# Kernel tuning notes

Hardware: AMD Instinct MI355X
Metric: run time of the kernel (lower is better)

## Reference

```python
import jax, jax.numpy as jnp
import numpy as np

B, T, V, E, H, O = 512, 64, 1024, 256, 512, 256


def setup_inputs() -> dict:
    key = jax.random.key(0)
    ks = jax.random.split(key, 9)
    s = 0.02
    return {
        "message": jax.random.normal(ks[0], (B, T, V), jnp.float32),
        "W_emb": jax.random.normal(ks[1], (E, V), jnp.float32) * s,   # Linear(vocab, embed).weight
        "b_emb": jnp.zeros((E,), jnp.float32),
        "W_ih": jax.random.normal(ks[2], (4 * H, E), jnp.float32) * s,  # LSTMCell weight_ih (i,f,g,o)
        "b_ih": jnp.zeros((4 * H,), jnp.float32),
        "W_hh": jax.random.normal(ks[3], (4 * H, H), jnp.float32) * s,  # LSTMCell weight_hh
        "b_hh": jnp.zeros((4 * H,), jnp.float32),
        "W_agent": jax.random.normal(ks[4], (O, H), jnp.float32) * s,   # agent Linear(hidden, out)
        "b_agent": jnp.zeros((O,), jnp.float32),
    }


def reference(message, W_emb, b_emb, W_ih, b_ih, W_hh, b_hh, W_agent, b_agent):
    # Embedding for all timesteps at once: [B,T,V] @ [E,V]^T -> [B,T,E]
    emb = jnp.einsum('btv,ev->bte', message, W_emb) + b_emb
    # Precompute input-side gate preactivations for every step: [B,T,4H]
    x_gates = jnp.einsum('bte,ge->btg', emb, W_ih) + (b_ih + b_hh)
    x_gates = jnp.swapaxes(x_gates, 0, 1)  # [T,B,4H] for scan
    Bsz = message.shape[0]
    Hh = W_hh.shape[1]

    def step(carry, xg):
        h, c = carry
        g = xg + h @ W_hh.T                      # [B,4H]
        i, f, gg, o = jnp.split(g, 4, axis=-1)   # PyTorch LSTMCell gate order i,f,g,o
        i = jax.nn.sigmoid(i)
        f = jax.nn.sigmoid(f)
        gg = jnp.tanh(gg)
        o = jax.nn.sigmoid(o)
        c = f * c + i * gg
        h = o * jnp.tanh(c)
        return (h, c), h

    h0 = jnp.zeros((Bsz, Hh), message.dtype)
    _, hs = jax.lax.scan(step, (h0, h0), x_gates)  # hs: [T,B,H]
    # Agent head applied to every step's hidden state, output [B,T,O]
    out = jnp.einsum('tbh,oh->bto', hs, W_agent) + b_agent
    return out
```

## Files before the change

kernel.cpp:

```cpp
#include <hip/hip_runtime.h>

typedef unsigned short u16;
typedef unsigned int u32;
typedef unsigned long long u64;
typedef __attribute__((ext_vector_type(8))) short bf16x8;
typedef __attribute__((ext_vector_type(4))) float f32x4;

__device__ inline u16 f2bf(float x) {
  u32 u = __float_as_uint(x);
  u32 r = (u + 0x7FFFu + ((u >> 16) & 1u)) >> 16;
  return (u16)r;
}
__device__ inline float bf2f(u16 h) { return __uint_as_float(((u32)h) << 16); }
__device__ inline float sigm(float x) { return 1.f / (1.f + __expf(-x)); }
__device__ inline float tanh_s(float x) {
  float ax = fabsf(x);
  float e = __expf(2.f * ax);
  float t = 1.f - 2.f / (e + 1.f);
  return copysignf(t, x);
}

__global__ void cvt_f32_bf16(const float* __restrict__ s, u16* __restrict__ d, int n) {
  int i = (blockIdx.x * 256 + threadIdx.x) * 4;
  if (i < n) {
    float4 f = *(const float4*)&s[i];
    u32 lo = (u32)f2bf(f.x) | ((u32)f2bf(f.y) << 16);
    u32 hi = (u32)f2bf(f.z) | ((u32)f2bf(f.w) << 16);
    uint2 v; v.x = lo; v.y = hi;
    *(uint2*)&d[i] = v;
  }
}

__global__ void bias_add(const float* __restrict__ a, const float* __restrict__ b,
                         float* __restrict__ d, int n) {
  int i = blockIdx.x * 256 + threadIdx.x;
  if (i < n) d[i] = a[i] + b[i];
}

__global__ void zero_u32(u32* __restrict__ p, int n) {
  int i = blockIdx.x * 256 + threadIdx.x;
  if (i < n) p[i] = 0;
}

template <int A_F32, int OUT_BF16>
__global__ __launch_bounds__(256) void gemm_bt(
    const void* __restrict__ Ap, const u16* __restrict__ Bp,
    const float* __restrict__ bias, void* __restrict__ Cp,
    int K, int lda, int ldb, int ldc) {
  __shared__ u16 Alds[128 * 64];
  __shared__ u16 Blds[128 * 64];
  const int tid = threadIdx.x;
  const int lane = tid & 63;
  const int w = tid >> 6;
  const int wm = w >> 1, wn = w & 1;
  const int m0 = blockIdx.x * 128, n0 = blockIdx.y * 128;
  const int r = lane & 15, kb = lane >> 4;

  f32x4 acc[4][4];
#pragma unroll
  for (int m = 0; m < 4; ++m)
#pragma unroll
    for (int n = 0; n < 4; ++n) acc[m][n] = (f32x4)0.f;

  for (int k0 = 0; k0 < K; k0 += 64) {
#pragma unroll
    for (int p = 0; p < 4; ++p) {
      int ch = p * 256 + tid;
      int row = ch >> 3;
      int col = (ch & 7) * 8;
      int scol = col ^ ((row & 7) << 3);
      if (A_F32) {
        const float* s = (const float*)Ap + (size_t)(m0 + row) * lda + k0 + col;
        float4 f0 = *(const float4*)s;
        float4 f1 = *(const float4*)(s + 4);
        uint4 v;
        v.x = (u32)f2bf(f0.x) | ((u32)f2bf(f0.y) << 16);
        v.y = (u32)f2bf(f0.z) | ((u32)f2bf(f0.w) << 16);
        v.z = (u32)f2bf(f1.x) | ((u32)f2bf(f1.y) << 16);
        v.w = (u32)f2bf(f1.z) | ((u32)f2bf(f1.w) << 16);
        *(uint4*)&Alds[row * 64 + scol] = v;
      } else {
        uint4 v = *(const uint4*)((const u16*)Ap + (size_t)(m0 + row) * lda + k0 + col);
        *(uint4*)&Alds[row * 64 + scol] = v;
      }
      uint4 vb = *(const uint4*)(Bp + (size_t)(n0 + row) * ldb + k0 + col);
      *(uint4*)&Blds[row * 64 + scol] = vb;
    }
    __syncthreads();
#pragma unroll
    for (int ks = 0; ks < 2; ++ks) {
      int kk = ks * 32 + kb * 8;
      bf16x8 af[4], bfr[4];
#pragma unroll
      for (int m = 0; m < 4; ++m) {
        int row = wm * 64 + m * 16 + r;
        af[m] = *(const bf16x8*)&Alds[row * 64 + (kk ^ ((row & 7) << 3))];
      }
#pragma unroll
      for (int n = 0; n < 4; ++n) {
        int row = wn * 64 + n * 16 + r;
        bfr[n] = *(const bf16x8*)&Blds[row * 64 + (kk ^ ((row & 7) << 3))];
      }
#pragma unroll
      for (int m = 0; m < 4; ++m)
#pragma unroll
        for (int n = 0; n < 4; ++n)
          acc[m][n] = __builtin_amdgcn_mfma_f32_16x16x32_bf16(af[m], bfr[n], acc[m][n], 0, 0, 0);
    }
    __syncthreads();
  }

  const int r4 = kb * 4;
#pragma unroll
  for (int m = 0; m < 4; ++m) {
#pragma unroll
    for (int n = 0; n < 4; ++n) {
      int row = m0 + wm * 64 + m * 16 + r4;
      int col = n0 + wn * 64 + n * 16 + (lane & 15);
      float bv = bias[col];
#pragma unroll
      for (int j = 0; j < 4; ++j) {
        float v = acc[m][n][j] + bv;
        if (OUT_BF16)
          ((u16*)Cp)[(size_t)(row + j) * ldc + col] = f2bf(v);
        else
          ((float*)Cp)[(size_t)(row + j) * ldc + col] = v;
      }
    }
  }
}

__global__ __launch_bounds__(256, 1) void lstm_persist(
    const u16* __restrict__ xg,
    const u16* __restrict__ Whh,
    u16* __restrict__ h2,
    u16* __restrict__ hs,
    u32* ctr) {
  const int tid = threadIdx.x;
  const int lane = tid & 63;
  const int w = tid >> 6;
  const int g = blockIdx.x & 7;
  const int m = blockIdx.x >> 3;
  const int b0 = g * 64;
  const int hc0 = m * 16;
  const int col = lane & 15;
  const int q = lane >> 4;

  float cst[4] = {0.f, 0.f, 0.f, 0.f};
  const int arow = b0 + w * 16 + col;
  const int gr0 = b0 + w * 16 + q * 4;

  for (int t = 0; t < 64; ++t) {
    float xv[4][4];
#pragma unroll
    for (int j = 0; j < 4; ++j) {
      const u16* xp = xg + ((size_t)(gr0 + j) * 64 + t) * 2048 + hc0 + col;
#pragma unroll
      for (int n = 0; n < 4; ++n) xv[n][j] = bf2f(xp[n * 512]);
    }

    f32x4 acc[4];
#pragma unroll
    for (int n = 0; n < 4; ++n) acc[n] = (f32x4)0.f;

    if (t > 0) {
      const u16* hp = h2 + (size_t)((t - 1) & 1) * (512 * 512) + (size_t)arow * 512;
#pragma unroll
      for (int kf = 0; kf < 16; ++kf) {
        union { u64 qq[2]; bf16x8 v; } ua;
        const u64* hq = (const u64*)&hp[kf * 32 + q * 8];
        ua.qq[0] = __hip_atomic_load(&hq[0], __ATOMIC_RELAXED, __HIP_MEMORY_SCOPE_AGENT);
        ua.qq[1] = __hip_atomic_load(&hq[1], __ATOMIC_RELAXED, __HIP_MEMORY_SCOPE_AGENT);
#pragma unroll
        for (int n = 0; n < 4; ++n) {
          bf16x8 bfr = *(const bf16x8*)&Whh[(size_t)(n * 512 + hc0 + col) * 512 + kf * 32 + q * 8];
          acc[n] = __builtin_amdgcn_mfma_f32_16x16x32_bf16(ua.v, bfr, acc[n], 0, 0, 0);
        }
      }
    }

    u16* hw = h2 + (size_t)(t & 1) * (512 * 512);
#pragma unroll
    for (int j = 0; j < 4; ++j) {
      float vi = acc[0][j] + xv[0][j];
      float vf = acc[1][j] + xv[1][j];
      float vg = acc[2][j] + xv[2][j];
      float vo = acc[3][j] + xv[3][j];
      float ii = sigm(vi), ff = sigm(vf), gg = tanh_s(vg), oo = sigm(vo);
      float cn = ff * cst[j] + ii * gg;
      cst[j] = cn;
      u16 hb = f2bf(oo * tanh_s(cn));
      int br = gr0 + j;
      __hip_atomic_store(&hw[(size_t)br * 512 + hc0 + col], hb,
                         __ATOMIC_RELAXED, __HIP_MEMORY_SCOPE_AGENT);
      hs[((size_t)br * 64 + t) * 512 + hc0 + col] = hb;
    }

    if (t < 63) {
      asm volatile("s_waitcnt vmcnt(0)" ::: "memory");
      __syncthreads();
      if (tid == 0) {
        u32* c = &ctr[(size_t)(t * 8 + g) * 32];
        __hip_atomic_fetch_add(c, 1u, __ATOMIC_RELAXED, __HIP_MEMORY_SCOPE_AGENT);
        while (__hip_atomic_load(c, __ATOMIC_RELAXED, __HIP_MEMORY_SCOPE_AGENT) < 32u)
          __builtin_amdgcn_s_sleep(2);
      }
      __syncthreads();
    }
  }
}

extern "C" void kernel_launch(void* const* d_in, const int* in_sizes, int n_in,
                              void* d_out, int out_size, void* d_ws, size_t ws_size,
                              hipStream_t stream) {
  (void)in_sizes; (void)n_in; (void)out_size; (void)ws_size;
  const float* msg   = (const float*)d_in[0];
  const float* W_emb = (const float*)d_in[1];
  const float* b_emb = (const float*)d_in[2];
  const float* W_ih  = (const float*)d_in[3];
  const float* b_ih  = (const float*)d_in[4];
  const float* W_hh  = (const float*)d_in[5];
  const float* b_hh  = (const float*)d_in[6];
  const float* W_ag  = (const float*)d_in[7];
  const float* b_ag  = (const float*)d_in[8];
  float* out = (float*)d_out;

  char* p = (char*)d_ws;
  u16* Wemb_b = (u16*)p;  p += (size_t)256 * 1024 * 2;
  u16* Wih_b  = (u16*)p;  p += (size_t)2048 * 256 * 2;
  u16* Whh_b  = (u16*)p;  p += (size_t)2048 * 512 * 2;
  u16* Wag_b  = (u16*)p;  p += (size_t)256 * 512 * 2;
  float* bc   = (float*)p; p += (size_t)2048 * 4;
  p = (char*)(((size_t)p + 255) & ~(size_t)255);
  u16* emb_b = (u16*)p;   p += (size_t)32768 * 256 * 2;
  u16* xg    = (u16*)p;   p += (size_t)32768 * 2048 * 2;
  u16* hs    = (u16*)p;   p += (size_t)32768 * 512 * 2;
  u16* h2    = (u16*)p;   p += (size_t)2 * 512 * 512 * 2;
  u32* ctr   = (u32*)p;   p += (size_t)64 * 8 * 32 * 4;

  cvt_f32_bf16<<<256, 256, 0, stream>>>(W_emb, Wemb_b, 256 * 1024);
  cvt_f32_bf16<<<512, 256, 0, stream>>>(W_ih, Wih_b, 2048 * 256);
  cvt_f32_bf16<<<1024, 256, 0, stream>>>(W_hh, Whh_b, 2048 * 512);
  cvt_f32_bf16<<<128, 256, 0, stream>>>(W_ag, Wag_b, 256 * 512);
  bias_add<<<8, 256, 0, stream>>>(b_ih, b_hh, bc, 2048);
  zero_u32<<<64, 256, 0, stream>>>(ctr, 64 * 8 * 32);

  gemm_bt<1, 1><<<dim3(256, 2), 256, 0, stream>>>(msg, Wemb_b, b_emb, emb_b,
                                                  1024, 1024, 1024, 256);
  gemm_bt<0, 1><<<dim3(256, 16), 256, 0, stream>>>(emb_b, Wih_b, bc, xg,
                                                   256, 256, 256, 2048);
  lstm_persist<<<256, 256, 0, stream>>>(xg, Whh_b, h2, hs, ctr);
  gemm_bt<0, 0><<<dim3(256, 2), 256, 0, stream>>>(hs, Wag_b, b_ag, out,
                                                  512, 512, 512, 256);
}
```

Measured before the change: 1.132 ms.

## Stage W_hh and h in swizzled LDS, time-major gate layout, prefetch xgates

After: 1.036 ms. 8.5% less time.

```diff
diff --git a/kernel.cpp b/kernel.cpp
--- a/kernel.cpp
+++ b/kernel.cpp
@@ -42,7 +42,7 @@
   if (i < n) p[i] = 0;
 }
 
-template <int A_F32, int OUT_BF16>
+template <int A_F32, int OUT_BF16, int ROWPERM>
 __global__ __launch_bounds__(256) void gemm_bt(
     const void* __restrict__ Ap, const u16* __restrict__ Bp,
     const float* __restrict__ bias, void* __restrict__ Cp,
@@ -121,21 +121,25 @@
 #pragma unroll
       for (int j = 0; j < 4; ++j) {
         float v = acc[m][n][j] + bv;
+        size_t crow = ROWPERM ? ((size_t)((row + j) & 63) * 512 + ((row + j) >> 6))
+                              : (size_t)(row + j);
         if (OUT_BF16)
-          ((u16*)Cp)[(size_t)(row + j) * ldc + col] = f2bf(v);
+          ((u16*)Cp)[crow * ldc + col] = f2bf(v);
         else
-          ((float*)Cp)[(size_t)(row + j) * ldc + col] = v;
+          ((float*)Cp)[crow * ldc + col] = v;
       }
     }
   }
 }
 
 __global__ __launch_bounds__(256, 1) void lstm_persist(
-    const u16* __restrict__ xg,
+    const u16* __restrict__ xgT,
     const u16* __restrict__ Whh,
     u16* __restrict__ h2,
     u16* __restrict__ hs,
     u32* ctr) {
+  __shared__ u16 Bl[64 * 512];
+  __shared__ u16 hA[64 * 512];
   const int tid = threadIdx.x;
   const int lane = tid & 63;
   const int w = tid >> 6;
@@ -143,60 +147,97 @@
   const int m = blockIdx.x >> 3;
   const int b0 = g * 64;
   const int hc0 = m * 16;
-  const int col = lane & 15;
-  const int q = lane >> 4;
-
-  float cst[4] = {0.f, 0.f, 0.f, 0.f};
-  const int arow = b0 + w * 16 + col;
-  const int gr0 = b0 + w * 16 + q * 4;
+  const int r = lane & 15, q = lane >> 4;
+
+  {
+    int row = tid >> 2;
+    int gg = row >> 4, cc = row & 15;
+    int c0 = (tid & 3) * 128;
+    const u16* src = Whh + (size_t)(gg * 512 + hc0 + cc) * 512 + c0;
+#pragma unroll
+    for (int i = 0; i < 16; ++i) {
+      int col = c0 + i * 8;
+      int scol = col ^ ((row & 7) << 3);
+      *(uint4*)&Bl[row * 512 + scol] = *(const uint4*)&src[i * 8];
+    }
+  }
+  __syncthreads();
+
+  float cstate[4] = {0.f, 0.f, 0.f, 0.f};
+  const int bl0 = b0 + w * 16 + q * 4;
+
+  u16 xv[4][4];
+#pragma unroll
+  for (int j = 0; j < 4; ++j) {
+    const u16* xp = xgT + (size_t)(bl0 + j) * 2048 + hc0 + r;
+#pragma unroll
+    for (int n = 0; n < 4; ++n) xv[j][n] = xp[n * 512];
+  }
 
   for (int t = 0; t < 64; ++t) {
-    float xv[4][4];
+    f32x4 acc[4];
+#pragma unroll
+    for (int n = 0; n < 4; ++n) acc[n] = (f32x4)0.f;
+
+    if (t > 0) {
+      {
+        int row = tid >> 2;
+        int c0 = (tid & 3) * 128;
+        const u64* src = (const u64*)(h2 + (size_t)((t - 1) & 1) * (512 * 512) +
+                                      (size_t)(b0 + row) * 512 + c0);
+        u64 tmp[32];
+#pragma unroll
+        for (int i = 0; i < 32; ++i)
+          tmp[i] = __hip_atomic_load(&src[i], __ATOMIC_RELAXED, __HIP_MEMORY_SCOPE_AGENT);
+#pragma unroll
+        for (int i = 0; i < 16; ++i) {
+          int col = c0 + i * 8;
+          int scol = col ^ ((row & 7) << 3);
+          u64* dst = (u64*)&hA[row * 512 + scol];
+          dst[0] = tmp[i * 2];
+          dst[1] = tmp[i * 2 + 1];
+        }
+      }
+      __syncthreads();
+
+#pragma unroll
+      for (int kf = 0; kf < 16; ++kf) {
+        int k = kf * 32 + q * 8;
+        int scol = k ^ ((r & 7) << 3);
+        bf16x8 a = *(const bf16x8*)&hA[(w * 16 + r) * 512 + scol];
+#pragma unroll
+        for (int n = 0; n < 4; ++n) {
+          bf16x8 b = *(const bf16x8*)&Bl[(n * 16 + r) * 512 + scol];
+          acc[n] = __builtin_amdgcn_mfma_f32_16x16x32_bf16(a, b, acc[n], 0, 0, 0);
+        }
+      }
+    }
+
+    u16* hw = h2 + (size_t)(t & 1) * (512 * 512);
 #pragma unroll
     for (int j = 0; j < 4; ++j) {
-      const u16* xp = xg + ((size_t)(gr0 + j) * 64 + t) * 2048 + hc0 + col;
-#pragma unroll
-      for (int n = 0; n < 4; ++n) xv[n][j] = bf2f(xp[n * 512]);
-    }
-
-    f32x4 acc[4];
-#pragma unroll
-    for (int n = 0; n < 4; ++n) acc[n] = (f32x4)0.f;
-
-    if (t > 0) {
-      const u16* hp = h2 + (size_t)((t - 1) & 1) * (512 * 512) + (size_t)arow * 512;
-#pragma unroll
-      for (int kf = 0; kf < 16; ++kf) {
-        union { u64 qq[2]; bf16x8 v; } ua;
-        const u64* hq = (const u64*)&hp[kf * 32 + q * 8];
-        ua.qq[0] = __hip_atomic_load(&hq[0], __ATOMIC_RELAXED, __HIP_MEMORY_SCOPE_AGENT);
-        ua.qq[1] = __hip_atomic_load(&hq[1], __ATOMIC_RELAXED, __HIP_MEMORY_SCOPE_AGENT);
-#pragma unroll
-        for (int n = 0; n < 4; ++n) {
-          bf16x8 bfr = *(const bf16x8*)&Whh[(size_t)(n * 512 + hc0 + col) * 512 + kf * 32 + q * 8];
-          acc[n] = __builtin_amdgcn_mfma_f32_16x16x32_bf16(ua.v, bfr, acc[n], 0, 0, 0);
-        }
-      }
-    }
-
-    u16* hw = h2 + (size_t)(t & 1) * (512 * 512);
-#pragma unroll
-    for (int j = 0; j < 4; ++j) {
-      float vi = acc[0][j] + xv[0][j];
-      float vf = acc[1][j] + xv[1][j];
-      float vg = acc[2][j] + xv[2][j];
-      float vo = acc[3][j] + xv[3][j];
+      float vi = acc[0][j] + bf2f(xv[j][0]);
+      float vf = acc[1][j] + bf2f(xv[j][1]);
+      float vg = acc[2][j] + bf2f(xv[j][2]);
+      float vo = acc[3][j] + bf2f(xv[j][3]);
       float ii = sigm(vi), ff = sigm(vf), gg = tanh_s(vg), oo = sigm(vo);
-      float cn = ff * cst[j] + ii * gg;
-      cst[j] = cn;
+      float cn = ff * cstate[j] + ii * gg;
+      cstate[j] = cn;
       u16 hb = f2bf(oo * tanh_s(cn));
-      int br = gr0 + j;
-      __hip_atomic_store(&hw[(size_t)br * 512 + hc0 + col], hb,
+      int br = bl0 + j;
+      __hip_atomic_store(&hw[(size_t)br * 512 + hc0 + r], hb,
                          __ATOMIC_RELAXED, __HIP_MEMORY_SCOPE_AGENT);
-      hs[((size_t)br * 64 + t) * 512 + hc0 + col] = hb;
+      hs[((size_t)br * 64 + t) * 512 + hc0 + r] = hb;
     }
 
     if (t < 63) {
+      const u16* xb2 = xgT + (size_t)(t + 1) * 512 * 2048;
+#pragma unroll
+      for (int j = 0; j < 4; ++j) {
+        const u16* xp = xb2 + (size_t)(bl0 + j) * 2048 + hc0 + r;
+#pragma unroll
+        for (int n = 0; n < 4; ++n) xv[j][n] = xp[n * 512];
+      }
       asm volatile("s_waitcnt vmcnt(0)" ::: "memory");
       __syncthreads();
       if (tid == 0) {
@@ -233,7 +274,7 @@
   float* bc   = (float*)p; p += (size_t)2048 * 4;
   p = (char*)(((size_t)p + 255) & ~(size_t)255);
   u16* emb_b = (u16*)p;   p += (size_t)32768 * 256 * 2;
-  u16* xg    = (u16*)p;   p += (size_t)32768 * 2048 * 2;
+  u16* xgT   = (u16*)p;   p += (size_t)32768 * 2048 * 2;
   u16* hs    = (u16*)p;   p += (size_t)32768 * 512 * 2;
   u16* h2    = (u16*)p;   p += (size_t)2 * 512 * 512 * 2;
   u32* ctr   = (u32*)p;   p += (size_t)64 * 8 * 32 * 4;
@@ -245,11 +286,11 @@
   bias_add<<<8, 256, 0, stream>>>(b_ih, b_hh, bc, 2048);
   zero_u32<<<64, 256, 0, stream>>>(ctr, 64 * 8 * 32);
 
-  gemm_bt<1, 1><<<dim3(256, 2), 256, 0, stream>>>(msg, Wemb_b, b_emb, emb_b,
-                                                  1024, 1024, 1024, 256);
-  gemm_bt<0, 1><<<dim3(256, 16), 256, 0, stream>>>(emb_b, Wih_b, bc, xg,
-                                                   256, 256, 256, 2048);
-  lstm_persist<<<256, 256, 0, stream>>>(xg, Whh_b, h2, hs, ctr);
-  gemm_bt<0, 0><<<dim3(256, 2), 256, 0, stream>>>(hs, Wag_b, b_ag, out,
-                                                  512, 512, 512, 256);
-}
+  gemm_bt<1, 1, 0><<<dim3(256, 2), 256, 0, stream>>>(msg, Wemb_b, b_emb, emb_b,
+                                                     1024, 1024, 1024, 256);
+  gemm_bt<0, 1, 1><<<dim3(256, 16), 256, 0, stream>>>(emb_b, Wih_b, bc, xgT,
+                                                      256, 256, 256, 2048);
+  lstm_persist<<<256, 256, 0, stream>>>(xgT, Whh_b, h2, hs, ctr);
+  gemm_bt<0, 0, 0><<<dim3(256, 2), 256, 0, stream>>>(hs, Wag_b, b_ag, out,
+                                                     512, 512, 512, 256);
+}
```
